# Performance work log

Hardware: AMD Instinct MI355X
Metric: run time of the kernel (lower is better)

The kernel has to match this reference:

```python
import jax, jax.numpy as jnp
import numpy as np

BN_EPS = 1e-5


def setup_inputs() -> dict:
    key = jax.random.key(0)
    ks = jax.random.split(key, 8)
    B, C, T, H, W = 8, 64, 16, 56, 56
    Cr = C // 4  # ratio=4 bottleneck in RouteFuncMLP
    s = lambda k, shape, scale=0.05: jax.random.normal(k, shape, jnp.float32) * scale
    return {
        "x": jax.random.normal(ks[0], (B, C, T, H, W), jnp.float32),
        "view": 3,  # View.FOUL
        "emb": s(ks[1], (4, C), 1.0),
        "Wg": s(ks[2], (C, C)),
        "bg": jnp.zeros((C,), jnp.float32),
        "Wa": s(ks[3], (Cr, C, 3)),
        "ba": jnp.zeros((Cr,), jnp.float32),
        "bn_gamma": jnp.ones((Cr,), jnp.float32),
        "bn_beta": jnp.zeros((Cr,), jnp.float32),
        "bn_mean": jnp.zeros((Cr,), jnp.float32),
        "bn_var": jnp.ones((Cr,), jnp.float32),
        "Wb": s(ks[4], (C, Cr, 3)),
        "Wconv": s(ks[5], (C, C, 3, 3)),
        "Wcls": s(ks[6], (10, C)),
        "bcls": jnp.zeros((10,), jnp.float32),
    }


def _conv1d_t(x, w, pad):
    # Temporal conv: x [B, Cin, T], w [Cout, Cin, K] -> [B, Cout, T]
    return jax.lax.conv_general_dilated(
        x, w, window_strides=(1,), padding=[(pad, pad)],
        dimension_numbers=("NCH", "OIH", "NCH"))


def _route_func(x, Wg, bg, Wa, ba, bn_gamma, bn_beta, bn_mean, bn_var, Wb):
    # RouteFuncMLP: per-frame, per-channel calibration factors. x: [B,C,T,H,W]
    g = x.mean(axis=(2, 3, 4))  # global pool -> [B,C]
    xt = x.mean(axis=(3, 4))    # spatial pool -> [B,C,T]
    g = jnp.einsum("oc,bc->bo", Wg, g) + bg  # 1x1x1 conv on global branch
    h = _conv1d_t(xt + g[:, :, None], Wa, pad=1) + ba[None, :, None]  # [B,Cr,T]
    # BatchNorm3d (inference form with running stats)
    h = (h - bn_mean[None, :, None]) * jax.lax.rsqrt(bn_var[None, :, None] + BN_EPS)
    h = h * bn_gamma[None, :, None] + bn_beta[None, :, None]
    h = jax.nn.relu(h)
    return _conv1d_t(h, Wb, pad=1) + 1.0  # alpha: [B,C,T]


def reference(x, view, emb, Wg, bg, Wa, ba, bn_gamma, bn_beta, bn_mean, bn_var, Wb, Wconv, Wcls, bcls):
    B, C, T, H, W = x.shape
    # embed-add: broadcast the view embedding over T,H,W
    x = x + emb[view][None, :, None, None, None]
    alpha = _route_func(x, Wg, bg, Wa, ba, bn_gamma, bn_beta, bn_mean, bn_var, Wb)
    # TAdaConv2d with cal_dim='cin': scaling the shared kernel per input channel
    # (per batch, per frame) is mathematically identical to scaling the input
    # channels first and convolving with the shared kernel.
    xs = x * alpha[:, :, :, None, None]
    xs = xs.transpose(0, 2, 1, 3, 4).reshape(B * T, C, H, W)
    y = jax.lax.conv_general_dilated(
        xs, Wconv, window_strides=(1, 1), padding=[(1, 1), (1, 1)],
        dimension_numbers=("NCHW", "OIHW", "NCHW"))
    y = y.reshape(B, T, C, H, W).transpose(0, 2, 1, 3, 4)  # [B,C,T,H,W]
    pooled = y.max(axis=(2, 3, 4))  # max over T,H,W -> [B,C]
    return pooled @ Wcls.T + bcls   # [B,10]
```

## Files before the change

### kernel.cpp

```cpp
#include <hip/hip_runtime.h>
#include <math.h>

#define B_ 8
#define C_ 64
#define T_ 16
#define H_ 56
#define W_ 56
#define HW_ (H_ * W_)
#define CR_ 16

typedef __attribute__((ext_vector_type(8))) short bf16x8;
typedef __attribute__((ext_vector_type(4))) float f32x4;

__device__ __forceinline__ void atomicMaxF(float* addr, float v) {
    if (v >= 0.f) atomicMax((int*)addr, __float_as_int(v));
    else          atomicMin((unsigned int*)addr, (unsigned int)__float_as_int(v));
}

__device__ __forceinline__ unsigned short f2bf(float f) {
    unsigned u = __float_as_uint(f);
    u += 0x7fffu + ((u >> 16) & 1u);
    return (unsigned short)(u >> 16);
}

__device__ __forceinline__ void gload_lds16(const void* g, void* l) {
    __builtin_amdgcn_global_load_lds(
        (const __attribute__((address_space(1))) unsigned int*)g,
        (__attribute__((address_space(3))) unsigned int*)l,
        16, 0, 0);
}

__global__ __launch_bounds__(256) void prep_kernel(
    const float* __restrict__ x, const float* __restrict__ emb,
    const int* __restrict__ viewp, unsigned short* __restrict__ xs,
    float* __restrict__ xt)
{
    __shared__ float sred[4][8];
    int blk = blockIdx.x;
    int ch = blk & 7, bt = blk >> 3;
    int b = bt >> 4, t = bt & 15;
    int tid = threadIdx.x, lane = tid & 63, wv = tid >> 6;
    int view = viewp[0];

    float e[8];
    #pragma unroll
    for (int j = 0; j < 8; ++j) e[j] = emb[view * C_ + ch * 8 + j];

    const float* xb = x + ((size_t)(b * C_ + ch * 8) * T_ + t) * HW_;
    unsigned short* xso = xs + ((size_t)bt * 8 + ch) * (58 * 58) * 8;

    for (int i = tid; i < 228; i += 256) {
        int r, c;
        if (i < 58)       { r = 0;            c = i; }
        else if (i < 116) { r = 57;           c = i - 58; }
        else if (i < 172) { r = i - 116 + 1;  c = 0; }
        else              { r = i - 172 + 1;  c = 57; }
        *(bf16x8*)(xso + ((size_t)r * 58 + c) * 8) = (bf16x8){0,0,0,0,0,0,0,0};
    }

    float psum[8];
    #pragma unroll
    for (int j = 0; j < 8; ++j) psum[j] = 0.f;

    for (int item = tid; item < 784; item += 256) {
        int row = item / 14, cg = item - row * 14;
        float4 f[8];
        #pragma unroll
        for (int j = 0; j < 8; ++j) {
            float4 v = *(const float4*)(xb + (size_t)j * (T_ * HW_) + item * 4);
            v.x += e[j]; v.y += e[j]; v.z += e[j]; v.w += e[j];
            psum[j] += (v.x + v.y) + (v.z + v.w);
            f[j] = v;
        }
        unsigned short* outp = xso + ((size_t)(row + 1) * 58 + cg * 4 + 1) * 8;
        #pragma unroll
        for (int cc = 0; cc < 4; ++cc) {
            const float* fc = (const float*)&f[0] + cc;
            bf16x8 hv;
            #pragma unroll
            for (int j = 0; j < 8; ++j)
                hv[j] = (short)f2bf(((const float4*)fc)[j].x);
            *(bf16x8*)(outp + cc * 8) = hv;
        }
    }

    #pragma unroll
    for (int j = 0; j < 8; ++j) {
        float s = psum[j];
        #pragma unroll
        for (int off = 32; off > 0; off >>= 1) s += __shfl_down(s, off);
        if (lane == 0) sred[wv][j] = s;
    }
    __syncthreads();
    if (tid < 8) {
        float s = sred[0][tid] + sred[1][tid] + sred[2][tid] + sred[3][tid];
        xt[((size_t)b * C_ + ch * 8 + tid) * T_ + t] = s;
    }
}

__global__ __launch_bounds__(256) void route_kernel(
    const float* __restrict__ xt,
    const float* __restrict__ Wg, const float* __restrict__ bg,
    const float* __restrict__ Wa, const float* __restrict__ ba,
    const float* __restrict__ bng, const float* __restrict__ bnb,
    const float* __restrict__ bnm, const float* __restrict__ bnv,
    const float* __restrict__ Wb, float* __restrict__ alphaT)
{
    __shared__ float swg[64 * 65];
    __shared__ float swa[64 * 48];
    __shared__ float swb[48 * 64];
    __shared__ float z[64 * 18];
    __shared__ float gs[64], ggs[64];
    __shared__ float hs[16][18];
    int b = blockIdx.x, tid = threadIdx.x;

    for (int idx = tid; idx < 4096; idx += 256) {
        int c = idx >> 6, i = idx & 63;
        swg[c * 65 + i] = Wg[idx];
    }
    for (int idx = tid; idx < 3072; idx += 256) {
        int r = idx / 192, rem = idx % 192;
        int i = rem / 3, tap = rem % 3;
        swa[i * 48 + r * 3 + tap] = Wa[idx];
    }
    for (int idx = tid; idx < 3072; idx += 256) {
        int k = idx >> 6, c = idx & 63;
        swb[idx] = Wb[c * 48 + k];
    }
    for (int idx = tid; idx < 1024; idx += 256) {
        int c = idx >> 4, t = idx & 15;
        z[c * 18 + t + 1] = xt[b * 1024 + idx] * (1.f / HW_);
    }
    if (tid < 64) { z[tid * 18] = 0.f; z[tid * 18 + 17] = 0.f; }
    if (tid < 16) { hs[tid][0] = 0.f; hs[tid][17] = 0.f; }
    __syncthreads();

    if (tid < 64) {
        float s = 0.f;
        #pragma unroll
        for (int t = 1; t <= 16; ++t) s += z[tid * 18 + t];
        gs[tid] = s * (1.f / 16.f);
    }
    __syncthreads();
    if (tid < 64) {
        float acc = bg[tid];
        #pragma unroll 8
        for (int i = 0; i < 64; ++i) acc = fmaf(swg[tid * 65 + i], gs[i], acc);
        ggs[tid] = acc;
    }
    __syncthreads();
    for (int idx = tid; idx < 1024; idx += 256) {
        int c = idx >> 4, t = idx & 15;
        z[c * 18 + t + 1] += ggs[c];
    }
    __syncthreads();

    {
        int t = tid >> 4, r = tid & 15;
        float v = ba[r];
        #pragma unroll 8
        for (int i = 0; i < 64; ++i) {
            const float* wa = &swa[i * 48 + r * 3];
            const float* zz = &z[i * 18 + t];
            v = fmaf(zz[0], wa[0], v);
            v = fmaf(zz[1], wa[1], v);
            v = fmaf(zz[2], wa[2], v);
        }
        v = (v - bnm[r]) * rsqrtf(bnv[r] + 1e-5f);
        v = fmaf(v, bng[r], bnb[r]);
        hs[r][t + 1] = fmaxf(v, 0.f);
    }
    __syncthreads();

    for (int idx = tid; idx < 1024; idx += 256) {
        int t = idx >> 6, c = idx & 63;
        float v = 1.f;
        #pragma unroll
        for (int r = 0; r < 16; ++r) {
            v = fmaf(hs[r][t],     swb[(r * 3 + 0) * 64 + c], v);
            v = fmaf(hs[r][t + 1], swb[(r * 3 + 1) * 64 + c], v);
            v = fmaf(hs[r][t + 2], swb[(r * 3 + 2) * 64 + c], v);
        }
        alphaT[(b * T_ + t) * C_ + c] = v;
    }
}

__global__ __launch_bounds__(256) void prepack_kernel(
    const float* __restrict__ Wconv, float* __restrict__ packW0,
    float* __restrict__ pooled)
{
    int idx = blockIdx.x * 256 + threadIdx.x;
    if (idx < 512) pooled[idx] = -INFINITY;
    if (idx >= 64 * 576) return;
    int j     = idx & 7;
    int lane  = (idx >> 3) & 63;
    int mt    = (idx >> 9) & 3;
    int kstep = idx >> 11;
    int cih = kstep & 1, tap = kstep >> 1;
    int co = mt * 16 + (lane & 15);
    int ci = cih * 32 + (lane >> 4) * 8 + j;
    packW0[idx] = Wconv[(co * C_ + ci) * 9 + tap];
}

__global__ __launch_bounds__(256) void wscale_kernel(
    const float* __restrict__ packW0, const float* __restrict__ alphaT,
    unsigned short* __restrict__ packWbt)
{
    __shared__ float sal[C_];
    int bt = blockIdx.x, tid = threadIdx.x;
    if (tid < C_) sal[tid] = alphaT[bt * C_ + tid];
    __syncthreads();
    for (int f = tid; f < 4608; f += 256) {
        int lane = f & 63, kstep = f >> 8;
        int cibase = (kstep & 1) * 32 + ((lane >> 4)) * 8;
        const float* w = packW0 + (size_t)f * 8;
        bf16x8 hv;
        #pragma unroll
        for (int j = 0; j < 8; ++j) hv[j] = (short)f2bf(w[j] * sal[cibase + j]);
        *(bf16x8*)(packWbt + (size_t)bt * 36864 + (size_t)f * 8) = hv;
    }
}

#define RROWS 8
#define LROWS2 10
#define LCOLS2 58
#define ROWE (8 * LCOLS2)

__global__ __launch_bounds__(256) void conv_mfma_kernel(
    const unsigned short* __restrict__ xs,
    const unsigned short* __restrict__ packWbt,
    float* __restrict__ pooled)
{
    __shared__ bf16x8 ltile[LROWS2 * ROWE];
    __shared__ float smax[4][C_];

    int blk = blockIdx.x;
    int strip = blk % 7;
    int bt = blk / 7;
    int b = bt >> 4;
    int h0 = strip * RROWS;
    int tid = threadIdx.x;
    int lane = tid & 63, wv = tid >> 6;

    const unsigned short* xsbt = xs + (size_t)bt * (8 * 3364 * 8);
    for (int s = wv; s < 80; s += 4) {
        int row = s >> 3, ch = s & 7;
        const unsigned short* src =
            xsbt + ((size_t)ch * 3364 + (size_t)(h0 + row) * 58 + lane) * 8;
        if (lane < 58)
            gload_lds16(src, &ltile[(row * 8 + ch) * LCOLS2]);
    }
    __syncthreads();

    int q = lane >> 4, li = lane & 15;
    int baddr[7];
    #pragma unroll
    for (int nt = 0; nt < 7; ++nt) {
        int p = (wv * 7 + nt) * 16 + li;
        int row = p / W_, col = p - row * W_;
        baddr[nt] = row * ROWE + q * LCOLS2 + col;
    }

    f32x4 acc[7][4];
    #pragma unroll
    for (int nt = 0; nt < 7; ++nt)
        #pragma unroll
        for (int mt = 0; mt < 4; ++mt)
            acc[nt][mt] = (f32x4){0.f, 0.f, 0.f, 0.f};

    const bf16x8* pw = (const bf16x8*)(packWbt + (size_t)bt * 36864);

    #pragma unroll
    for (int kh = 0; kh < 3; ++kh) {
        #pragma unroll
        for (int kw = 0; kw < 3; ++kw) {
            #pragma unroll
            for (int cih = 0; cih < 2; ++cih) {
                const int kstep = (kh * 3 + kw) * 2 + cih;
                const int boff = kh * ROWE + kw + cih * (4 * LCOLS2);
                bf16x8 af[4];
                #pragma unroll
                for (int mt = 0; mt < 4; ++mt)
                    af[mt] = pw[(kstep * 4 + mt) * 64 + lane];
                #pragma unroll
                for (int nt = 0; nt < 7; ++nt) {
                    bf16x8 bfr = ltile[baddr[nt] + boff];
                    #pragma unroll
                    for (int mt = 0; mt < 4; ++mt)
                        acc[nt][mt] = __builtin_amdgcn_mfma_f32_16x16x32_bf16(
                            af[mt], bfr, acc[nt][mt], 0, 0, 0);
                }
            }
        }
    }

    float m[4][4];
    #pragma unroll
    for (int mt = 0; mt < 4; ++mt)
        #pragma unroll
        for (int i = 0; i < 4; ++i) {
            float v = acc[0][mt][i];
            #pragma unroll
            for (int nt = 1; nt < 7; ++nt) v = fmaxf(v, acc[nt][mt][i]);
            m[mt][i] = v;
        }
    #pragma unroll
    for (int off = 1; off < 16; off <<= 1)
        #pragma unroll
        for (int mt = 0; mt < 4; ++mt)
            #pragma unroll
            for (int i = 0; i < 4; ++i)
                m[mt][i] = fmaxf(m[mt][i], __shfl_xor(m[mt][i], off));
    if (li == 0) {
        #pragma unroll
        for (int mt = 0; mt < 4; ++mt)
            #pragma unroll
            for (int i = 0; i < 4; ++i)
                smax[wv][mt * 16 + q * 4 + i] = m[mt][i];
    }
    __syncthreads();
    if (tid < C_) {
        float mm = fmaxf(fmaxf(smax[0][tid], smax[1][tid]),
                         fmaxf(smax[2][tid], smax[3][tid]));
        atomicMaxF(&pooled[b * C_ + tid], mm);
    }
}

__global__ void cls_kernel(const float* __restrict__ pooled,
                           const float* __restrict__ Wcls,
                           const float* __restrict__ bcls,
                           float* __restrict__ out)
{
    int i = threadIdx.x;
    if (i >= B_ * 10) return;
    int b = i / 10, k = i % 10;
    float v = bcls[k];
    for (int c = 0; c < C_; ++c) v = fmaf(pooled[b * C_ + c], Wcls[k * C_ + c], v);
    out[i] = v;
}

extern "C" void kernel_launch(void* const* d_in, const int* in_sizes, int n_in,
                              void* d_out, int out_size, void* d_ws, size_t ws_size,
                              hipStream_t stream)
{
    const float* x     = (const float*)d_in[0];
    const int*   view  = (const int*)  d_in[1];
    const float* emb   = (const float*)d_in[2];
    const float* Wg    = (const float*)d_in[3];
    const float* bg    = (const float*)d_in[4];
    const float* Wa    = (const float*)d_in[5];
    const float* ba    = (const float*)d_in[6];
    const float* bng   = (const float*)d_in[7];
    const float* bnb   = (const float*)d_in[8];
    const float* bnm   = (const float*)d_in[9];
    const float* bnv   = (const float*)d_in[10];
    const float* Wb    = (const float*)d_in[11];
    const float* Wconv = (const float*)d_in[12];
    const float* Wcls  = (const float*)d_in[13];
    const float* bcls  = (const float*)d_in[14];
    float* out = (float*)d_out;

    char* wsb = (char*)d_ws;
    float*          xt      = (float*)(wsb + 0);
    float*          alphaT  = (float*)(wsb + 32768);
    float*          pooled  = (float*)(wsb + 65536);
    float*          packW0  = (float*)(wsb + 67584);
    unsigned short* packWbt = (unsigned short*)(wsb + 215040);
    unsigned short* xs      = (unsigned short*)(wsb + 9652224);

    hipLaunchKernelGGL(prepack_kernel, dim3(144), dim3(256), 0, stream,
                       Wconv, packW0, pooled);
    hipLaunchKernelGGL(prep_kernel, dim3(1024), dim3(256), 0, stream,
                       x, emb, view, xs, xt);
    hipLaunchKernelGGL(route_kernel, dim3(B_), dim3(256), 0, stream,
                       xt, Wg, bg, Wa, ba, bng, bnb, bnm, bnv, Wb, alphaT);
    hipLaunchKernelGGL(wscale_kernel, dim3(B_ * T_), dim3(256), 0, stream,
                       packW0, alphaT, packWbt);
    hipLaunchKernelGGL(conv_mfma_kernel, dim3(B_ * T_ * 7), dim3(256), 0, stream,
                       xs, packWbt, pooled);
    hipLaunchKernelGGL(cls_kernel, dim3(1), dim3(128), 0, stream, pooled, Wcls, bcls, out);
}
```

Measured before the change: 98.01 us.

## Split prep kernel into row-group blocks with atomic partial-sum reduction

The prep kernel now launches seven times as many blocks, each with 128 threads. Each block handles 8 rows of one (b,t,channel-group) slice in a single pass instead of a loop over 784 items. Per-block partial spatial sums are combined into xt with atomicAdd, so xt is zeroed in the prepack kernel. This is meant to raise parallelism and memory-level concurrency in the bandwidth-bound layout and bf16 conversion pass. The cost is more blocks, float atomics whose summation order varies, and 16 idle threads per block.

After: 98.91 us. Within noise of the previous version (+0.9%).

```diff
diff --git a/kernel.cpp b/kernel.cpp
--- a/kernel.cpp
+++ b/kernel.cpp
@@ -30,14 +30,34 @@
         16, 0, 0);
 }
 
-__global__ __launch_bounds__(256) void prep_kernel(
+__global__ __launch_bounds__(256) void prepack_kernel(
+    const float* __restrict__ Wconv, float* __restrict__ packW0,
+    float* __restrict__ pooled, float* __restrict__ xt)
+{
+    int idx = blockIdx.x * 256 + threadIdx.x;
+    if (idx < 512) pooled[idx] = -INFINITY;
+    if (idx < 8192) xt[idx] = 0.f;
+    if (idx >= 64 * 576) return;
+    int j     = idx & 7;
+    int lane  = (idx >> 3) & 63;
+    int mt    = (idx >> 9) & 3;
+    int kstep = idx >> 11;
+    int cih = kstep & 1, tap = kstep >> 1;
+    int co = mt * 16 + (lane & 15);
+    int ci = cih * 32 + (lane >> 4) * 8 + j;
+    packW0[idx] = Wconv[(co * C_ + ci) * 9 + tap];
+}
+
+__global__ __launch_bounds__(128) void prep_kernel(
     const float* __restrict__ x, const float* __restrict__ emb,
     const int* __restrict__ viewp, unsigned short* __restrict__ xs,
     float* __restrict__ xt)
 {
-    __shared__ float sred[4][8];
+    __shared__ float sred[2][8];
     int blk = blockIdx.x;
-    int ch = blk & 7, bt = blk >> 3;
+    int g  = blk % 7;
+    int ch = (blk / 7) & 7;
+    int bt = blk / 56;
     int b = bt >> 4, t = bt & 15;
     int tid = threadIdx.x, lane = tid & 63, wv = tid >> 6;
     int view = viewp[0];
@@ -49,37 +69,43 @@
     const float* xb = x + ((size_t)(b * C_ + ch * 8) * T_ + t) * HW_;
     unsigned short* xso = xs + ((size_t)bt * 8 + ch) * (58 * 58) * 8;
 
-    for (int i = tid; i < 228; i += 256) {
-        int r, c;
-        if (i < 58)       { r = 0;            c = i; }
-        else if (i < 116) { r = 57;           c = i - 58; }
-        else if (i < 172) { r = i - 116 + 1;  c = 0; }
-        else              { r = i - 172 + 1;  c = 57; }
-        *(bf16x8*)(xso + ((size_t)r * 58 + c) * 8) = (bf16x8){0,0,0,0,0,0,0,0};
+    if (g == 0) {
+        for (int i = tid; i < 228; i += 128) {
+            int r, c;
+            if (i < 58)       { r = 0;            c = i; }
+            else if (i < 116) { r = 57;           c = i - 58; }
+            else if (i < 172) { r = i - 116 + 1;  c = 0; }
+            else              { r = i - 172 + 1;  c = 57; }
+            *(bf16x8*)(xso + ((size_t)r * 58 + c) * 8) = (bf16x8){0,0,0,0,0,0,0,0};
+        }
     }
 
     float psum[8];
     #pragma unroll
     for (int j = 0; j < 8; ++j) psum[j] = 0.f;
 
-    for (int item = tid; item < 784; item += 256) {
-        int row = item / 14, cg = item - row * 14;
+    if (tid < 112) {
+        int rl = tid / 14, cg = tid - rl * 14;
+        int row = g * 8 + rl;
+        int item = row * 14 + cg;
         float4 f[8];
         #pragma unroll
         for (int j = 0; j < 8; ++j) {
             float4 v = *(const float4*)(xb + (size_t)j * (T_ * HW_) + item * 4);
             v.x += e[j]; v.y += e[j]; v.z += e[j]; v.w += e[j];
-            psum[j] += (v.x + v.y) + (v.z + v.w);
+            psum[j] = (v.x + v.y) + (v.z + v.w);
             f[j] = v;
         }
         unsigned short* outp = xso + ((size_t)(row + 1) * 58 + cg * 4 + 1) * 8;
         #pragma unroll
         for (int cc = 0; cc < 4; ++cc) {
-            const float* fc = (const float*)&f[0] + cc;
             bf16x8 hv;
             #pragma unroll
-            for (int j = 0; j < 8; ++j)
-                hv[j] = (short)f2bf(((const float4*)fc)[j].x);
+            for (int j = 0; j < 8; ++j) {
+                float comp = (cc == 0) ? f[j].x : (cc == 1) ? f[j].y
+                           : (cc == 2) ? f[j].z : f[j].w;
+                hv[j] = (short)f2bf(comp);
+            }
             *(bf16x8*)(outp + cc * 8) = hv;
         }
     }
@@ -93,8 +119,8 @@
     }
     __syncthreads();
     if (tid < 8) {
-        float s = sred[0][tid] + sred[1][tid] + sred[2][tid] + sred[3][tid];
-        xt[((size_t)b * C_ + ch * 8 + tid) * T_ + t] = s;
+        float s = sred[0][tid] + sred[1][tid];
+        atomicAdd(&xt[((size_t)b * C_ + ch * 8 + tid) * T_ + t], s);
     }
 }
 
@@ -183,23 +209,6 @@
         }
         alphaT[(b * T_ + t) * C_ + c] = v;
     }
-}
-
-__global__ __launch_bounds__(256) void prepack_kernel(
-    const float* __restrict__ Wconv, float* __restrict__ packW0,
-    float* __restrict__ pooled)
-{
-    int idx = blockIdx.x * 256 + threadIdx.x;
-    if (idx < 512) pooled[idx] = -INFINITY;
-    if (idx >= 64 * 576) return;
-    int j     = idx & 7;
-    int lane  = (idx >> 3) & 63;
-    int mt    = (idx >> 9) & 3;
-    int kstep = idx >> 11;
-    int cih = kstep & 1, tap = kstep >> 1;
-    int co = mt * 16 + (lane & 15);
-    int ci = cih * 32 + (lane >> 4) * 8 + j;
-    packW0[idx] = Wconv[(co * C_ + ci) * 9 + tap];
 }
 
 __global__ __launch_bounds__(256) void wscale_kernel(
@@ -369,8 +378,8 @@
     unsigned short* xs      = (unsigned short*)(wsb + 9652224);
 
     hipLaunchKernelGGL(prepack_kernel, dim3(144), dim3(256), 0, stream,
-                       Wconv, packW0, pooled);
-    hipLaunchKernelGGL(prep_kernel, dim3(1024), dim3(256), 0, stream,
+                       Wconv, packW0, pooled, xt);
+    hipLaunchKernelGGL(prep_kernel, dim3(B_ * T_ * 8 * 7), dim3(128), 0, stream,
                        x, emb, view, xs, xt);
     hipLaunchKernelGGL(route_kernel, dim3(B_), dim3(256), 0, stream,
                        xt, Wg, bg, Wa, ba, bng, bnb, bnm, bnv, Wb, alphaT);
```
